# Kernel tuning notes

Measured on AMD Instinct MI355X. Metric: run time of the kernel, lower is better.

## Reference

```python
import jax, jax.numpy as jnp
import numpy as np

B, F0, D = 2048, 39, 16
CROSS = [200, 200, 200]


def setup_inputs() -> dict:
    key = jax.random.key(0)
    ks = jax.random.split(key, 7)
    inp = {"x": jax.random.normal(ks[0], (B, F0, D), dtype=jnp.float32)}
    prev = F0
    for i, c in enumerate(CROSS):
        # Conv1d(in=F0*prev, out=c, kernel=1) weight reshaped to (c, F0, prev)
        scale = 1.0 / np.sqrt(F0 * prev)
        inp[f"W{i}"] = jax.random.normal(ks[1 + 2 * i], (c, F0, prev), dtype=jnp.float32) * scale
        inp[f"b{i}"] = jnp.zeros((c,), dtype=jnp.float32)
        prev = c
    return inp


def reference(x, W0, b0, W1, b1, W2, b2):
    # x: (B, F0, D). Each CIN layer in torch materializes x0*h -> (B, F0*prev, D)
    # then applies a kernel-1 Conv1d. Mathematically this is the bilinear
    # contraction below (same values, no quadratic intermediate).
    x0 = x
    h = x
    xs = []
    for W, b in ((W0, b0), (W1, b1), (W2, b2)):
        # z[b,o,d] = sum_{f,g} W[o,f,g] * x0[b,f,d] * h[b,g,d] + bias[o]
        z = jnp.einsum('bfd,bgd,ofg->bod', x0, h, W) + b[None, :, None]
        h = jax.nn.relu(z)
        xs.append(h)
    # concat over channel dim, sum-pool over embed dim -> (B, sum(cross_sizes))
    return jnp.sum(jnp.concatenate(xs, axis=1), axis=2)
```

## Files before the change

kernel.cpp:

```cpp
#include <hip/hip_runtime.h>
#include <hip/hip_bf16.h>
#include <stdint.h>

typedef __attribute__((ext_vector_type(8))) short bf16x8;
typedef __attribute__((ext_vector_type(4))) float f32x4;
typedef unsigned short u16;
typedef unsigned int u32;

#define GLL(gp, lp) __builtin_amdgcn_global_load_lds( \
    (const __attribute__((address_space(1))) void*)(gp), \
    (__attribute__((address_space(3))) void*)(lp), 16, 0, 0)

__device__ __forceinline__ u16 f2bf_rne(float v) {
    u32 u = __float_as_uint(v);
    u32 r = (u + 0x7fffu + ((u >> 16) & 1u)) >> 16;
    return (u16)r;
}


__global__ void pack_x_kernel(const float* __restrict__ x, u16* __restrict__ xbd) {
    int idx = blockIdx.x * 256 + threadIdx.x;
    if (idx >= 32768 * 40) return;
    int m = idx / 40, f = idx - m * 40;
    int b = m >> 4, d = m & 15;
    float v = (f < 39) ? x[(b * 39 + f) * 16 + d] : 0.0f;
    xbd[idx] = f2bf_rne(v);
}

__global__ void pack_w0_kernel(const float* __restrict__ W, u16* __restrict__ Wp) {
    int idx = blockIdx.x * 256 + threadIdx.x;
    if (idx >= 224 * 1600) return;
    int o = idx / 1600, k = idx - o * 1600;
    int f = k / 40, g = k - f * 40;
    float v = (o < 200 && f < 39 && g < 39) ? W[(o * 39 + f) * 39 + g] : 0.0f;
    Wp[idx] = f2bf_rne(v);
}

__global__ void pack_w12_kernel(const float* __restrict__ W, u16* __restrict__ Wp) {
    int idx = blockIdx.x * 256 + threadIdx.x;
    if (idx >= 224 * 8128) return;
    int o = idx / 8128, k = idx - o * 8128;
    int f = k / 208, g = k - f * 208;
    float v = (o < 200 && f < 39 && g < 200) ? W[o * 7800 + f * 200 + g] : 0.0f;
    Wp[idx] = f2bf_rne(v);
}

template <int LAYER>
__global__ __launch_bounds__(512, 2) void cin_gemm3(
    const u16* __restrict__ Xbd,
    const u16* __restrict__ Hin,
    const u16* __restrict__ Wp,
    const float* __restrict__ bias,
    u16* __restrict__ Hout,
    float* __restrict__ out)
{
    constexpr int KP    = (LAYER == 0) ? 1600 : 8128;
    constexpr int NPAIR = KP / 64;
    constexpr u32 MAGIC = (LAYER == 0) ? 3277u : 10083u;
    constexpr int SHIFT = (LAYER == 0) ? 17 : 21;
    constexpr int GS    = (LAYER == 0) ? 40 : 208;
    constexpr int HROW  = (LAYER == 0) ? 40 : 208;
    constexpr int HSZ   = (LAYER == 0) ? 0 : 106496;
    constexpr int WOFF  = 20480 + HSZ;
    constexpr int SMEMA = WOFF + 28672;
    constexpr int SMEM  = (SMEMA > 117760) ? SMEMA : 117760;

    __shared__ __align__(16) char smem[SMEM];
    u16* Xl = (u16*)smem;
    u16* Hl = (u16*)(smem + 20480);

    const int bid  = blockIdx.x;
    const int mblk = bid >> 1, nblk = bid & 1;
    const int m0    = mblk * 256;
    const int ncol0 = nblk * 112;
    const int NT    = nblk ? 6 : 7;
    const int tid  = threadIdx.x;
    const int lane = tid & 63, wid = tid >> 6;
    const int mg = wid & 3, kg = wid >> 2;
    const int rowl = lane & 15, grp = lane >> 4;

    int goff0, goff1;
    {
        int u = wid * 64 + lane;
        int c = (u >= 448) ? 1 : 0;
        int uu = u - c * 448;
        goff0 = (ncol0 + (uu >> 2)) * KP + c * 32 + (uu & 3) * 8;
        int u1 = (wid + 8) * 64 + lane;
        int uu1 = u1 - 448;
        goff1 = (ncol0 + (uu1 >> 2)) * KP + 32 + (uu1 & 3) * 8;
    }

    {
        const char* xsrc = (const char*)(Xbd + (size_t)m0 * 40);
        for (int i = wid; i < 20; i += 8)
            GLL(xsrc + i * 1024 + lane * 16, smem + i * 1024);
    }
    if constexpr (LAYER > 0) {
        const char* hsrc = (const char*)(Hin + (size_t)m0 * 208);
        for (int i = wid; i < 104; i += 8)
            GLL(hsrc + i * 1024 + lane * 16, smem + 20480 + i * 1024);
    }
    {
        const u16* gsrc = Wp;
        char* wb = smem + WOFF;
        GLL((const char*)(gsrc + goff0), wb + wid * 1024);
        if (wid < 6) GLL((const char*)(gsrc + goff1), wb + wid * 1024 + 8192);
    }

    int xro[4], hro[4];
    #pragma unroll
    for (int s = 0; s < 4; ++s) {
        int r = mg * 64 + s * 16 + rowl;
        xro[s] = r * 40;
        hro[s] = r * HROW;
    }
    const u16* Hb = (LAYER == 0) ? Xl : Hl;

    f32x4 acc[4][7];
    #pragma unroll
    for (int s = 0; s < 4; ++s)
        #pragma unroll
        for (int t = 0; t < 7; ++t) {
            f32x4 z = {0.f, 0.f, 0.f, 0.f};
            acc[s][t] = z;
        }

    for (int pr = 0; pr < NPAIR; ++pr) {
        __syncthreads();
        if (pr + 1 < NPAIR) {
            const u16* gsrc = Wp + (size_t)(pr + 1) * 64;
            char* wb = smem + WOFF + ((pr + 1) & 1) * 14336;
            GLL((const char*)(gsrc + goff0), wb + wid * 1024);
            if (wid < 6) GLL((const char*)(gsrc + goff1), wb + wid * 1024 + 8192);
        }
        int k0 = pr * 64 + kg * 32 + grp * 8;
        u32 f = ((u32)k0 * MAGIC) >> SHIFT;
        int g0 = k0 - (int)f * GS;
        bf16x8 afrag[4];
        #pragma unroll
        for (int s = 0; s < 4; ++s) {
            u16 xs = Xl[xro[s] + (int)f];
            bf16x8 hv = *(const bf16x8*)&Hb[hro[s] + g0];
            float xf = __uint_as_float(((u32)xs) << 16);
            union { bf16x8 v; u32 w[4]; } hu, au;
            hu.v = hv;
            #pragma unroll
            for (int j = 0; j < 4; ++j) {
                float lo = __uint_as_float(hu.w[j] << 16);
                float hi = __uint_as_float(hu.w[j] & 0xffff0000u);
                float pl = xf * lo;
                float ph = xf * hi;
                u32 pk;
                asm("v_cvt_pk_bf16_f32 %0, %1, %2" : "=v"(pk) : "v"(pl), "v"(ph));
                au.w[j] = pk;
            }
            afrag[s] = au.v;
        }
        const u16* wbR = (const u16*)(smem + WOFF + (pr & 1) * 14336) + kg * 3584 + rowl * 32 + grp * 8;
        #pragma unroll
        for (int t = 0; t < 7; ++t) {
            if (t < NT) {
                bf16x8 bfrag = *(const bf16x8*)&wbR[t * 512];
                #pragma unroll
                for (int s = 0; s < 4; ++s)
                    acc[s][t] = __builtin_amdgcn_mfma_f32_16x16x32_bf16(afrag[s], bfrag, acc[s][t], 0, 0, 0);
            }
        }
    }

    __syncthreads();
    float* red = (float*)smem;
    const int rbase = mg * 7168 + lane * 4;
    if (kg == 1) {
        #pragma unroll
        for (int s = 0; s < 4; ++s)
            #pragma unroll
            for (int t = 0; t < 7; ++t)
                if (t < NT)
                    *(f32x4*)&red[rbase + (s * 7 + t) * 256] = acc[s][t];
    }
    __syncthreads();

    if (kg == 0) {
        float bias_t[7];
        #pragma unroll
        for (int t = 0; t < 7; ++t) {
            int oc = ncol0 + t * 16 + rowl;
            bias_t[t] = (t < NT && oc < 200) ? bias[oc] : 0.0f;
        }
        #pragma unroll
        for (int s = 0; s < 4; ++s) {
            int mrow0 = m0 + mg * 64 + s * 16;
            int bidx = mrow0 >> 4;
            #pragma unroll
            for (int t = 0; t < 7; ++t) {
                if (t < NT) {
                    int oc = ncol0 + t * 16 + rowl;
                    f32x4 o = *(const f32x4*)&red[rbase + (s * 7 + t) * 256];
                    f32x4 v = acc[s][t];
                    float h0 = fmaxf(v[0] + o[0] + bias_t[t], 0.0f);
                    float h1 = fmaxf(v[1] + o[1] + bias_t[t], 0.0f);
                    float h2 = fmaxf(v[2] + o[2] + bias_t[t], 0.0f);
                    float h3 = fmaxf(v[3] + o[3] + bias_t[t], 0.0f);
                    if constexpr (LAYER < 2) {
                        size_t rb = (size_t)(mrow0 + grp * 4) * 208 + oc;
                        Hout[rb]           = f2bf_rne(h0);
                        Hout[rb + 208]     = f2bf_rne(h1);
                        Hout[rb + 2*208]   = f2bf_rne(h2);
                        Hout[rb + 3*208]   = f2bf_rne(h3);
                    }
                    float ssum = (h0 + h1) + (h2 + h3);
                    ssum += __shfl_xor(ssum, 16);
                    ssum += __shfl_xor(ssum, 32);
                    if (grp == 0 && oc < 200)
                        out[(size_t)bidx * 600 + LAYER * 200 + oc] = ssum;
                }
            }
        }
    }
}

extern "C" void kernel_launch(void* const* d_in, const int* in_sizes, int n_in,
                              void* d_out, int out_size, void* d_ws, size_t ws_size,
                              hipStream_t stream) {
    const float* x  = (const float*)d_in[0];
    const float* W0 = (const float*)d_in[1];
    const float* b0 = (const float*)d_in[2];
    const float* W1 = (const float*)d_in[3];
    const float* b1 = (const float*)d_in[4];
    const float* W2 = (const float*)d_in[5];
    const float* b2 = (const float*)d_in[6];
    float* out = (float*)d_out;

    char* ws = (char*)d_ws;
    u16* xbd = (u16*)(ws);
    u16* wp0 = (u16*)(ws + 2621440);
    u16* wp1 = (u16*)(ws + 3338240);
    u16* wp2 = (u16*)(ws + 6979584);
    u16* h1  = (u16*)(ws + 10620928);
    u16* h2  = (u16*)(ws + 24252416);

    pack_x_kernel<<<5120, 256, 0, stream>>>(x, xbd);
    pack_w0_kernel<<<1400, 256, 0, stream>>>(W0, wp0);
    pack_w12_kernel<<<7112, 256, 0, stream>>>(W1, wp1);
    pack_w12_kernel<<<7112, 256, 0, stream>>>(W2, wp2);

    cin_gemm3<0><<<256, 512, 0, stream>>>(xbd, (const u16*)nullptr, wp0, b0, h1, out);
    cin_gemm3<1><<<256, 512, 0, stream>>>(xbd, h1, wp1, b1, h2, out);
    cin_gemm3<2><<<256, 512, 0, stream>>>(xbd, h2, wp2, b2, (u16*)nullptr, out);
}
```

Before: 292.4 us.

## Stream hidden state from global, enlarge weight K-stage to 256 with padded K

Stops staging the whole hidden-state tile (about 104 KB) in LDS and instead reads H fragments straight from global memory/cache. The freed LDS goes to a larger double-buffered weight stage covering 256 K per barrier instead of 64, which cuts the number of barriers. K is padded up to a multiple of 256, with f clamped so the padded region stays in range. The cost is more global/L2 traffic for H reads inside the inner loop, and some extra zero work from the padding.

```diff
diff --git a/kernel.cpp b/kernel.cpp
--- a/kernel.cpp
+++ b/kernel.cpp
@@ -29,8 +29,8 @@
 
 __global__ void pack_w0_kernel(const float* __restrict__ W, u16* __restrict__ Wp) {
     int idx = blockIdx.x * 256 + threadIdx.x;
-    if (idx >= 224 * 1600) return;
-    int o = idx / 1600, k = idx - o * 1600;
+    if (idx >= 224 * 1792) return;
+    int o = idx / 1792, k = idx - o * 1792;
     int f = k / 40, g = k - f * 40;
     float v = (o < 200 && f < 39 && g < 39) ? W[(o * 39 + f) * 39 + g] : 0.0f;
     Wp[idx] = f2bf_rne(v);
@@ -38,36 +38,33 @@
 
 __global__ void pack_w12_kernel(const float* __restrict__ W, u16* __restrict__ Wp) {
     int idx = blockIdx.x * 256 + threadIdx.x;
-    if (idx >= 224 * 8128) return;
-    int o = idx / 8128, k = idx - o * 8128;
+    if (idx >= 224 * 8192) return;
+    int o = idx / 8192, k = idx - o * 8192;
     int f = k / 208, g = k - f * 208;
     float v = (o < 200 && f < 39 && g < 200) ? W[o * 7800 + f * 200 + g] : 0.0f;
     Wp[idx] = f2bf_rne(v);
 }
 
 template <int LAYER>
-__global__ __launch_bounds__(512, 2) void cin_gemm3(
+__global__ __launch_bounds__(512, 2) void cin_gemm4(
     const u16* __restrict__ Xbd,
-    const u16* __restrict__ Hin,
+    const u16* __restrict__ Hglb,
     const u16* __restrict__ Wp,
     const float* __restrict__ bias,
     u16* __restrict__ Hout,
     float* __restrict__ out)
 {
-    constexpr int KP    = (LAYER == 0) ? 1600 : 8128;
-    constexpr int NPAIR = KP / 64;
-    constexpr u32 MAGIC = (LAYER == 0) ? 3277u : 10083u;
-    constexpr int SHIFT = (LAYER == 0) ? 17 : 21;
-    constexpr int GS    = (LAYER == 0) ? 40 : 208;
-    constexpr int HROW  = (LAYER == 0) ? 40 : 208;
-    constexpr int HSZ   = (LAYER == 0) ? 0 : 106496;
-    constexpr int WOFF  = 20480 + HSZ;
-    constexpr int SMEMA = WOFF + 28672;
-    constexpr int SMEM  = (SMEMA > 117760) ? SMEMA : 117760;
-
-    __shared__ __align__(16) char smem[SMEM];
+    constexpr int KP     = (LAYER == 0) ? 1792 : 8192;
+    constexpr int NGROUP = KP / 256;
+    constexpr u32 MAGIC  = (LAYER == 0) ? 3277u : 10083u;
+    constexpr int SHIFT  = (LAYER == 0) ? 17 : 21;
+    constexpr int GS     = (LAYER == 0) ? 40 : 208;
+    constexpr int HROW   = (LAYER == 0) ? 40 : 208;
+    constexpr int WOFF   = 20480;
+    constexpr int WBUF   = 57344;
+
+    __shared__ __align__(16) char smem[WOFF + 2 * WBUF];
     u16* Xl = (u16*)smem;
-    u16* Hl = (u16*)(smem + 20480);
 
     const int bid  = blockIdx.x;
     const int mblk = bid >> 1, nblk = bid & 1;
@@ -79,42 +76,27 @@
     const int mg = wid & 3, kg = wid >> 2;
     const int rowl = lane & 15, grp = lane >> 4;
 
-    int goff0, goff1;
-    {
-        int u = wid * 64 + lane;
-        int c = (u >= 448) ? 1 : 0;
-        int uu = u - c * 448;
-        goff0 = (ncol0 + (uu >> 2)) * KP + c * 32 + (uu & 3) * 8;
-        int u1 = (wid + 8) * 64 + lane;
-        int uu1 = u1 - 448;
-        goff1 = (ncol0 + (uu1 >> 2)) * KP + 32 + (uu1 & 3) * 8;
-    }
-
     {
         const char* xsrc = (const char*)(Xbd + (size_t)m0 * 40);
         for (int i = wid; i < 20; i += 8)
             GLL(xsrc + i * 1024 + lane * 16, smem + i * 1024);
     }
-    if constexpr (LAYER > 0) {
-        const char* hsrc = (const char*)(Hin + (size_t)m0 * 208);
-        for (int i = wid; i < 104; i += 8)
-            GLL(hsrc + i * 1024 + lane * 16, smem + 20480 + i * 1024);
-    }
+    const size_t wlsrc = (size_t)(ncol0 + (lane >> 2)) * KP + wid * 32 + (lane & 3) * 8;
     {
-        const u16* gsrc = Wp;
-        char* wb = smem + WOFF;
-        GLL((const char*)(gsrc + goff0), wb + wid * 1024);
-        if (wid < 6) GLL((const char*)(gsrc + goff1), wb + wid * 1024 + 8192);
-    }
-
-    int xro[4], hro[4];
+        char* wb = smem + WOFF + wid * 7168;
+        #pragma unroll
+        for (int j = 0; j < 7; ++j)
+            GLL((const char*)(Wp + wlsrc + (size_t)j * 16 * KP), wb + j * 1024);
+    }
+
+    int xro[4];
+    size_t hrg[4];
     #pragma unroll
     for (int s = 0; s < 4; ++s) {
         int r = mg * 64 + s * 16 + rowl;
         xro[s] = r * 40;
-        hro[s] = r * HROW;
-    }
-    const u16* Hb = (LAYER == 0) ? Xl : Hl;
+        hrg[s] = (size_t)(m0 + r) * HROW;
+    }
 
     f32x4 acc[4][7];
     #pragma unroll
@@ -125,45 +107,51 @@
             acc[s][t] = z;
         }
 
-    for (int pr = 0; pr < NPAIR; ++pr) {
+    for (int g = 0; g < NGROUP; ++g) {
         __syncthreads();
-        if (pr + 1 < NPAIR) {
-            const u16* gsrc = Wp + (size_t)(pr + 1) * 64;
-            char* wb = smem + WOFF + ((pr + 1) & 1) * 14336;
-            GLL((const char*)(gsrc + goff0), wb + wid * 1024);
-            if (wid < 6) GLL((const char*)(gsrc + goff1), wb + wid * 1024 + 8192);
-        }
-        int k0 = pr * 64 + kg * 32 + grp * 8;
-        u32 f = ((u32)k0 * MAGIC) >> SHIFT;
-        int g0 = k0 - (int)f * GS;
-        bf16x8 afrag[4];
-        #pragma unroll
-        for (int s = 0; s < 4; ++s) {
-            u16 xs = Xl[xro[s] + (int)f];
-            bf16x8 hv = *(const bf16x8*)&Hb[hro[s] + g0];
-            float xf = __uint_as_float(((u32)xs) << 16);
-            union { bf16x8 v; u32 w[4]; } hu, au;
-            hu.v = hv;
-            #pragma unroll
-            for (int j = 0; j < 4; ++j) {
-                float lo = __uint_as_float(hu.w[j] << 16);
-                float hi = __uint_as_float(hu.w[j] & 0xffff0000u);
-                float pl = xf * lo;
-                float ph = xf * hi;
-                u32 pk;
-                asm("v_cvt_pk_bf16_f32 %0, %1, %2" : "=v"(pk) : "v"(pl), "v"(ph));
-                au.w[j] = pk;
+        if (g + 1 < NGROUP) {
+            char* wb = smem + WOFF + ((g + 1) & 1) * WBUF + wid * 7168;
+            const u16* gsrc = Wp + wlsrc + (size_t)(g + 1) * 256;
+            #pragma unroll
+            for (int j = 0; j < 7; ++j)
+                GLL((const char*)(gsrc + (size_t)j * 16 * KP), wb + j * 1024);
+        }
+        const u16* wbase = (const u16*)(smem + WOFF + (g & 1) * WBUF);
+        #pragma unroll
+        for (int p = 0; p < 4; ++p) {
+            int k0 = g * 256 + p * 64 + kg * 32 + grp * 8;
+            u32 f = ((u32)k0 * MAGIC) >> SHIFT;
+            f = (f > 39u) ? 39u : f;
+            int g0 = k0 - (int)f * GS;
+            bf16x8 afrag[4];
+            #pragma unroll
+            for (int s = 0; s < 4; ++s) {
+                u16 xs = Xl[xro[s] + (int)f];
+                bf16x8 hv = *(const bf16x8*)(Hglb + hrg[s] + g0);
+                float xf = __uint_as_float(((u32)xs) << 16);
+                union { bf16x8 v; u32 w[4]; } hu, au;
+                hu.v = hv;
+                #pragma unroll
+                for (int j = 0; j < 4; ++j) {
+                    float lo = __uint_as_float(hu.w[j] << 16);
+                    float hi = __uint_as_float(hu.w[j] & 0xffff0000u);
+                    float pl = xf * lo;
+                    float ph = xf * hi;
+                    u32 pk;
+                    asm("v_cvt_pk_bf16_f32 %0, %1, %2" : "=v"(pk) : "v"(pl), "v"(ph));
+                    au.w[j] = pk;
+                }
+                afrag[s] = au.v;
             }
-            afrag[s] = au.v;
-        }
-        const u16* wbR = (const u16*)(smem + WOFF + (pr & 1) * 14336) + kg * 3584 + rowl * 32 + grp * 8;
-        #pragma unroll
-        for (int t = 0; t < 7; ++t) {
-            if (t < NT) {
-                bf16x8 bfrag = *(const bf16x8*)&wbR[t * 512];
-                #pragma unroll
-                for (int s = 0; s < 4; ++s)
-                    acc[s][t] = __builtin_amdgcn_mfma_f32_16x16x32_bf16(afrag[s], bfrag, acc[s][t], 0, 0, 0);
+            const u16* wbR = wbase + (p * 2 + kg) * 3584 + rowl * 32 + grp * 8;
+            #pragma unroll
+            for (int t = 0; t < 7; ++t) {
+                if (t < NT) {
+                    bf16x8 bfrag = *(const bf16x8*)&wbR[t * 512];
+                    #pragma unroll
+                    for (int s = 0; s < 4; ++s)
+                        acc[s][t] = __builtin_amdgcn_mfma_f32_16x16x32_bf16(afrag[s], bfrag, acc[s][t], 0, 0, 0);
+                }
             }
         }
     }
@@ -234,18 +222,18 @@
 
     char* ws = (char*)d_ws;
     u16* xbd = (u16*)(ws);
-    u16* wp0 = (u16*)(ws + 2621440);
-    u16* wp1 = (u16*)(ws + 3338240);
-    u16* wp2 = (u16*)(ws + 6979584);
-    u16* h1  = (u16*)(ws + 10620928);
-    u16* h2  = (u16*)(ws + 24252416);
+    u16* wp0 = (u16*)(ws + 2622464);
+    u16* wp1 = (u16*)(ws + 3425280);
+    u16* wp2 = (u16*)(ws + 7095296);
+    u16* h1  = (u16*)(ws + 10765312);
+    u16* h2  = (u16*)(ws + 24397824);
 
     pack_x_kernel<<<5120, 256, 0, stream>>>(x, xbd);
-    pack_w0_kernel<<<1400, 256, 0, stream>>>(W0, wp0);
-    pack_w12_kernel<<<7112, 256, 0, stream>>>(W1, wp1);
-    pack_w12_kernel<<<7112, 256, 0, stream>>>(W2, wp2);
-
-    cin_gemm3<0><<<256, 512, 0, stream>>>(xbd, (const u16*)nullptr, wp0, b0, h1, out);
-    cin_gemm3<1><<<256, 512, 0, stream>>>(xbd, h1, wp1, b1, h2, out);
-    cin_gemm3<2><<<256, 512, 0, stream>>>(xbd, h2, wp2, b2, (u16*)nullptr, out);
-}
+    pack_w0_kernel<<<1568, 256, 0, stream>>>(W0, wp0);
+    pack_w12_kernel<<<7168, 256, 0, stream>>>(W1, wp1);
+    pack_w12_kernel<<<7168, 256, 0, stream>>>(W2, wp2);
+
+    cin_gemm4<0><<<256, 512, 0, stream>>>(xbd, xbd, wp0, b0, h1, out);
+    cin_gemm4<1><<<256, 512, 0, stream>>>(xbd, h1, wp1, b1, h2, out);
+    cin_gemm4<2><<<256, 512, 0, stream>>>(xbd, h2, wp2, b2, (u16*)nullptr, out);
+}
```

New measurement: 342.4 us. +17.1%, slower.
